# Performance work log

Measured on AMD Instinct MI355X. Metric: run time of the kernel, lower is better.

The kernel has to match this reference:

```python
import jax, jax.numpy as jnp
import numpy as np
from jax import lax

SUB_NO = 20; T_NO = 200; BASIS_NO = 19; T_DATA = 100000; E_NO = 800; I_NO = 200


def make_cos_basis():
    # raised-cosine log-time basis, [BASIS_NO, T_NO]
    i = jnp.arange(BASIS_NO, dtype=jnp.float32)[:, None]
    phi = (jnp.pi / 2.0) * i
    x = jnp.arange(T_NO, dtype=jnp.float32)[None, :]
    raw = 5.0 * jnp.log(x + 1.0)  # cos_scale=5, cos_shift=1
    basis = 0.5 * jnp.cos(raw - phi) + 0.5
    return jnp.where((raw >= phi - jnp.pi) & (raw <= phi + jnp.pi), basis, 0.0)


def causal_group_conv(x, kern):
    # x: [T, sub], kern: [sub, T_no]; out[t,k] = sum_j kern[k,j]*x[t-j,k]
    xr = x.T[None]  # [1, sub, T]
    w = jnp.flip(kern, 1)[:, None, :]  # [sub, 1, T_no]
    out = lax.conv_general_dilated(xr, w, (1,), [(T_NO - 1, 0)],
                                   dimension_numbers=('NCH', 'OIH', 'NCH'),
                                   feature_group_count=kern.shape[0])
    return out[0].T  # [T, sub]


def hist_conv(z, kern):
    # matches torch: pad T_no leading zeros, valid corr with flipped kernel, drop last
    zp = jnp.concatenate([jnp.zeros((T_NO,), z.dtype), z])[None, None, :]
    w = jnp.flip(kern)[None, None, :]
    out = lax.conv_general_dilated(zp, w, (1,), 'VALID',
                                   dimension_numbers=('NCH', 'OIH', 'NCH'))
    return out[0, 0, :-1]  # [T]


def setup_inputs() -> dict:
    key = jax.random.key(0)
    ks = jax.random.split(key, 12)
    # binary dendritic tree: parent of node j is (j-1)//2; C_den[p, j] = 1
    parent = np.maximum((np.arange(SUB_NO) - 1) // 2, 0)
    C_den = np.zeros((SUB_NO, SUB_NO), np.float32)
    for j in range(1, SUB_NO):
        C_den[parent[j], j] = 1.0
    assign_e = jax.random.randint(ks[0], (E_NO,), 0, SUB_NO)
    assign_i = jax.random.randint(ks[1], (I_NO,), 0, SUB_NO)
    C_syn_e = jax.nn.one_hot(assign_e, SUB_NO, dtype=jnp.float32).T
    C_syn_i = jax.nn.one_hot(assign_i, SUB_NO, dtype=jnp.float32).T
    S_e = (jax.random.uniform(ks[2], (T_DATA, E_NO)) < 0.05).astype(jnp.float32)
    S_i = (jax.random.uniform(ks[3], (T_DATA, I_NO)) < 0.05).astype(jnp.float32)
    Z = (jax.random.uniform(ks[4], (T_DATA,)) < 0.02).astype(jnp.float32)
    return {
        'S_e': S_e, 'S_i': S_i, 'Z': Z,
        'C_den': jnp.asarray(C_den), 'C_syn_e': C_syn_e, 'C_syn_i': C_syn_i,
        'W_syn_ns': 0.1 * jax.random.normal(ks[5], (SUB_NO, BASIS_NO, 2)),
        'W_syn_s': 0.1 * jax.random.normal(ks[6], (SUB_NO, BASIS_NO, 2)),
        'W_sub_ns': 0.1 * jnp.ones((SUB_NO,), jnp.float32),
        'W_sub_s': 0.1 * jnp.ones((SUB_NO,), jnp.float32),
        'V_o': jax.random.normal(ks[7], (1,)),
        'Theta_ns': 0.1 * jax.random.normal(ks[8], (SUB_NO,)),
        'Theta_s': 0.1 * jax.random.normal(ks[9], (SUB_NO,)),
        'hist_s_weights': 0.1 * jax.random.normal(ks[10], (BASIS_NO,)),
        'hist_ns_weights': 0.1 * jax.random.normal(ks[11], (BASIS_NO,)),
    }


def reference(S_e, S_i, Z, C_den, C_syn_e, C_syn_i, W_syn_ns, W_syn_s,
              W_sub_ns, W_sub_s, V_o, Theta_ns, Theta_s,
              hist_s_weights, hist_ns_weights):
    cb = make_cos_basis()
    syn_e = S_e @ C_syn_e.T  # [T, sub]
    syn_i = S_i @ C_syn_i.T
    e_kern_ns = W_syn_ns[:, :, 0] @ cb  # [sub, T_no]
    i_kern_ns = W_syn_ns[:, :, 1] @ cb
    e_kern_s = W_syn_s[:, :, 0] @ cb
    i_kern_s = W_syn_s[:, :, 1] @ cb
    syn_ns = causal_group_conv(syn_e, e_kern_ns) + causal_group_conv(syn_i, i_kern_ns)
    syn_s = causal_group_conv(syn_e, e_kern_s) + causal_group_conv(syn_i, i_kern_s)
    ws2 = W_sub_s ** 2
    wns2 = W_sub_ns ** 2
    T = S_e.shape[0]
    s_out = jnp.zeros((T, SUB_NO), syn_s.dtype)
    ns_out = jnp.zeros((T, SUB_NO), syn_ns.dtype)
    # leaf-to-root tree message passing; C_den[k] masks children of node k
    for k in range(SUB_NO - 1, 0, -1):
        mask = C_den[k]
        s_out = s_out.at[:, k].set(jnp.tanh(syn_s[:, k] + s_out @ (mask * ws2) + Theta_s[k]))
        ns_out = ns_out.at[:, k].set(jnp.tanh(syn_ns[:, k] + ns_out @ (mask * wns2) + Theta_ns[k]))
    hist_s_kern = hist_s_weights @ cb  # [T_no]
    hist_ns_kern = hist_ns_weights @ cb
    root_mask = C_den[0]
    final_Z = jax.nn.sigmoid(hist_conv(Z, hist_s_kern) + syn_s[:, 0]
                             + s_out @ (root_mask * ws2) + Theta_s[0])
    root_ns = jnp.tanh(hist_conv(Z, hist_ns_kern) + syn_ns[:, 0]
                       + ns_out @ (root_mask * wns2) + Theta_ns[0])
    final_V = root_ns * wns2[0] + V_o[0]
    out_filters = jnp.vstack([e_kern_ns, i_kern_ns, e_kern_s, i_kern_s,
                              hist_ns_kern[None], hist_s_kern[None]])
    return final_V, final_Z, out_filters
```

## Files before the change

### kernel.cpp

```cpp
#include <hip/hip_runtime.h>
#include <hip/hip_bf16.h>
#include <math.h>

#define SUB_NO 20
#define T_NO   200
#define BASIS_NO 19
#define T_DATA 100000
#define E_NO   800
#define I_NO   200

using u16 = unsigned short;
using u32 = unsigned int;
using u64 = unsigned long long;

__device__ __forceinline__ float bf2f(u16 h) {
  return __builtin_bit_cast(float, (u32)h << 16);
}
__device__ __forceinline__ u16 f2bf(float f) {
  u32 u = __builtin_bit_cast(u32, f);
  u += 0x7FFFu + ((u >> 16) & 1u);
  return (u16)(u >> 16);
}
__device__ __forceinline__ float ldx(const void* p, int i, bool bf) {
  return bf ? bf2f(((const u16*)p)[i]) : ((const float*)p)[i];
}
__device__ __forceinline__ void stx(void* p, int i, float v, bool bf) {
  if (bf) ((u16*)p)[i] = f2bf(v); else ((float*)p)[i] = v;
}

#if defined(__clang__) && (__clang_major__ >= 17) && __has_builtin(__builtin_amdgcn_fdot2_f32_bf16)
typedef __bf16 bf16x2 __attribute__((ext_vector_type(2)));
__device__ __forceinline__ float dot2bf(u32 a, u32 b, float c) {
  return __builtin_amdgcn_fdot2_f32_bf16(__builtin_bit_cast(bf16x2, a),
                                         __builtin_bit_cast(bf16x2, b), c, false);
}
#else
__device__ __forceinline__ float dot2bf(u32 a, u32 b, float c) {
  float ax = __builtin_bit_cast(float, a << 16);
  float ay = __builtin_bit_cast(float, a & 0xFFFF0000u);
  float bx = __builtin_bit_cast(float, b << 16);
  float by = __builtin_bit_cast(float, b & 0xFFFF0000u);
  return fmaf(ay, by, fmaf(ax, bx, c));
}
#endif

#define K0_BLOCKS 21
__global__ __launch_bounds__(256) void k0_prep(
    const u32* __restrict__ probe,
    const void* __restrict__ Wns, const void* __restrict__ Ws,
    const void* __restrict__ hsw, const void* __restrict__ hnsw,
    const void* __restrict__ Cse, const void* __restrict__ Csi,
    u32* __restrict__ kpair, float* __restrict__ hist_s,
    float* __restrict__ hist_ns, int* __restrict__ ae, int* __restrict__ ai,
    void* __restrict__ out) {
  const bool bf = (probe[0] != 0u);
  __shared__ float cb[BASIS_NO * T_NO];
  const int tid = threadIdx.x;
  constexpr float PI = 3.14159265358979323846f;
  for (int idx = tid; idx < BASIS_NO * T_NO; idx += 256) {
    int b = idx / T_NO, j = idx - b * T_NO;
    float phi = 0.5f * PI * (float)b;
    float raw = 5.0f * logf((float)j + 1.0f);
    float v = 0.f;
    if (raw >= phi - PI && raw <= phi + PI) v = 0.5f * cosf(raw - phi) + 0.5f;
    cb[idx] = v;
  }
  __syncthreads();
  const int fbase = 2 * T_DATA;
  for (int gid = blockIdx.x * 256 + tid; gid < 5200; gid += K0_BLOCKS * 256) {
    if (gid < 4000) {
      int k = gid / T_NO, j = gid - k * T_NO;
      float e_ns = 0.f, i_ns = 0.f, e_s = 0.f, i_s = 0.f;
#pragma unroll
      for (int b = 0; b < BASIS_NO; ++b) {
        float c = cb[b * T_NO + j];
        e_ns = fmaf(ldx(Wns, (k * BASIS_NO + b) * 2 + 0, bf), c, e_ns);
        i_ns = fmaf(ldx(Wns, (k * BASIS_NO + b) * 2 + 1, bf), c, i_ns);
        e_s  = fmaf(ldx(Ws,  (k * BASIS_NO + b) * 2 + 0, bf), c, e_s);
        i_s  = fmaf(ldx(Ws,  (k * BASIS_NO + b) * 2 + 1, bf), c, i_s);
      }
      kpair[j * 40 + k]      = (u32)f2bf(e_ns) | ((u32)f2bf(i_ns) << 16);
      kpair[j * 40 + 20 + k] = (u32)f2bf(e_s)  | ((u32)f2bf(i_s)  << 16);
      stx(out, fbase + (0 * SUB_NO + k) * T_NO + j, e_ns, bf);
      stx(out, fbase + (1 * SUB_NO + k) * T_NO + j, i_ns, bf);
      stx(out, fbase + (2 * SUB_NO + k) * T_NO + j, e_s,  bf);
      stx(out, fbase + (3 * SUB_NO + k) * T_NO + j, i_s,  bf);
    } else if (gid < 4200) {
      int j = gid - 4000;
      float hs = 0.f, hns = 0.f;
#pragma unroll
      for (int b = 0; b < BASIS_NO; ++b) {
        float c = cb[b * T_NO + j];
        hs  = fmaf(ldx(hsw,  b, bf), c, hs);
        hns = fmaf(ldx(hnsw, b, bf), c, hns);
      }
      hist_s[j] = hs; hist_ns[j] = hns;
      stx(out, fbase + 80 * T_NO + j, hns, bf);
      stx(out, fbase + 81 * T_NO + j, hs,  bf);
    } else if (gid < 5000) {
      int e = gid - 4200;
      int a = 0;
      for (int k = 0; k < SUB_NO; ++k) if (ldx(Cse, k * E_NO + e, bf) != 0.f) a = k;
      ae[e] = a;
    } else {
      int e = gid - 5000;
      int a = 0;
      for (int k = 0; k < SUB_NO; ++k) if (ldx(Csi, k * I_NO + e, bf) != 0.f) a = k;
      ai[e] = a;
    }
  }
}

#define K1_R 64

__device__ __forceinline__ void k1_load_bf(const void* Se, const void* Si,
                                           int t, int l, uint4& a0, uint4& a1,
                                           uint4& c0) {
  const uint4 z4 = make_uint4(0u, 0u, 0u, 0u);
  const uint4* p = (const uint4*)((const u16*)Se + (size_t)t * E_NO);
  a0 = p[l]; a1 = (l < 36) ? p[64 + l] : z4;
  const uint4* pi = (const uint4*)((const u16*)Si + (size_t)t * I_NO);
  c0 = (l < 25) ? pi[l] : z4;
}

__device__ __forceinline__ void k1_proc_bf(uint4 a0, uint4 a1, uint4 c0,
                                           const u64* rme, const u64* rmi,
                                           int l, int t,
                                           u32* __restrict__ syn_pair) {
  u32 ce = 0, ci = 0;
#pragma unroll
  for (int j = 0; j < 8; ++j) {
    u32 d = (&a0.x)[j >> 1];
    u32 h = (j & 1) ? (d >> 16) : (d & 0xFFFFu);
    u64 m = __ballot(h != 0u);
    ce += (u32)__popcll(rme[j] & m);
  }
#pragma unroll
  for (int j = 0; j < 8; ++j) {
    u32 d = (&a1.x)[j >> 1];
    u32 h = (j & 1) ? (d >> 16) : (d & 0xFFFFu);
    u64 m = __ballot(h != 0u);
    ce += (u32)__popcll(rme[8 + j] & m);
  }
#pragma unroll
  for (int j = 0; j < 8; ++j) {
    u32 d = (&c0.x)[j >> 1];
    u32 h = (j & 1) ? (d >> 16) : (d & 0xFFFFu);
    u64 m = __ballot(h != 0u);
    ci += (u32)__popcll(rmi[j] & m);
  }
  if (l < SUB_NO) {
    u32 pe = (u32)f2bf((float)ce);
    u32 pif = (u32)f2bf((float)ci);
    syn_pair[(size_t)t * SUB_NO + l] = pe | (pif << 16);
  }
}

__global__ __launch_bounds__(256, 4) void k1_agg(
    const u32* __restrict__ probe,
    const void* __restrict__ Se, const void* __restrict__ Si,
    const int* __restrict__ ae, const int* __restrict__ ai,
    u32* __restrict__ syn_pair) {
  const bool bf = (probe[0] != 0u);
  __shared__ u64 mask_e[SUB_NO][16];
  __shared__ u64 mask_i[SUB_NO][8];
  __shared__ int lae[E_NO];
  __shared__ int lai[I_NO];
  const int tid = threadIdx.x;
  const int l = tid & 63;
  const int wv = tid >> 6;
  for (int n = tid; n < E_NO; n += 256) lae[n] = ae[n];
  for (int n = tid; n < I_NO; n += 256) lai[n] = ai[n];
  __syncthreads();
  for (int pid = tid; pid < 480; pid += 256) {
    if (pid < 320) {
      int k = pid >> 4, w = pid & 15;
      u64 m = 0;
      if (bf) {
        if (w < 8) { for (int b = 0; b < 64; ++b) if (lae[8 * b + w] == k) m |= 1ull << b; }
        else       { for (int b = 0; b < 36; ++b) if (lae[512 + 8 * b + (w - 8)] == k) m |= 1ull << b; }
      } else {
        int g = w >> 2, j = w & 3;
        int lim = (g < 3) ? 64 : 8;
        for (int b = 0; b < lim; ++b) if (lae[256 * g + 4 * b + j] == k) m |= 1ull << b;
      }
      mask_e[k][w] = m;
    } else {
      int p2 = pid - 320; int k = p2 >> 3, w = p2 & 7;
      u64 m = 0;
      if (bf) { for (int b = 0; b < 25; ++b) { int e = 8 * b + w; if (e < I_NO && lai[e] == k) m |= 1ull << b; } }
      else if (w < 4) { for (int b = 0; b < 50; ++b) if (lai[4 * b + w] == k) m |= 1ull << b; }
      mask_i[k][w] = m;
    }
  }
  __syncthreads();
  u64 rme[16], rmi[8];
  const int kk = (l < SUB_NO) ? l : 0;
#pragma unroll
  for (int w = 0; w < 16; ++w) rme[w] = mask_e[kk][w];
#pragma unroll
  for (int w = 0; w < 8; ++w) rmi[w] = mask_i[kk][w];

  const int r0 = blockIdx.x * K1_R + wv * 16;
  if (r0 >= T_DATA) return;
  const uint4 z4 = make_uint4(0u, 0u, 0u, 0u);

  if (bf) {
    uint4 A0, A1, C0, B0, B1, D0;
    k1_load_bf(Se, Si, r0, l, A0, A1, C0);
    k1_load_bf(Se, Si, r0 + 1, l, B0, B1, D0);
    for (int i = 0; i < 16; i += 2) {
      uint4 N0 = z4, N1 = z4, M0 = z4, M1 = z4, P0 = z4, Q0 = z4;
      if (i + 2 < 16) {
        k1_load_bf(Se, Si, r0 + i + 2, l, N0, N1, P0);
        k1_load_bf(Se, Si, r0 + i + 3, l, M0, M1, Q0);
      }
      k1_proc_bf(A0, A1, C0, rme, rmi, l, r0 + i, syn_pair);
      k1_proc_bf(B0, B1, D0, rme, rmi, l, r0 + i + 1, syn_pair);
      A0 = N0; A1 = N1; C0 = P0;
      B0 = M0; B1 = M1; D0 = Q0;
    }
  } else {
    uint4 a0, a1, a2, a3, c0;
    {
      const uint4* p = (const uint4*)((const float*)Se + (size_t)r0 * E_NO);
      a0 = p[l]; a1 = p[64 + l]; a2 = p[128 + l]; a3 = (l < 8) ? p[192 + l] : z4;
      const uint4* pi = (const uint4*)((const float*)Si + (size_t)r0 * I_NO);
      c0 = (l < 50) ? pi[l] : z4;
    }
    for (int i = 0; i < 16; ++i) {
      const int t = r0 + i;
      uint4 b0 = z4, b1 = z4, b2 = z4, b3 = z4, d0 = z4;
      if (i + 1 < 16) {
        const uint4* p = (const uint4*)((const float*)Se + (size_t)(t + 1) * E_NO);
        b0 = p[l]; b1 = p[64 + l]; b2 = p[128 + l]; b3 = (l < 8) ? p[192 + l] : z4;
        const uint4* pi = (const uint4*)((const float*)Si + (size_t)(t + 1) * I_NO);
        d0 = (l < 50) ? pi[l] : z4;
      }
      u32 ce = 0, ci = 0;
      const uint4 va[4] = {a0, a1, a2, a3};
#pragma unroll
      for (int g = 0; g < 4; ++g) {
#pragma unroll
        for (int j = 0; j < 4; ++j) {
          u32 d = (&va[g].x)[j];
          u64 m = __ballot(d != 0u);
          ce += (u32)__popcll(rme[4 * g + j] & m);
        }
      }
#pragma unroll
      for (int j = 0; j < 4; ++j) {
        u32 d = (&c0.x)[j];
        u64 m = __ballot(d != 0u);
        ci += (u32)__popcll(rmi[j] & m);
      }
      if (l < SUB_NO) {
        u32 pe = (u32)f2bf((float)ce);
        u32 pif = (u32)f2bf((float)ci);
        syn_pair[(size_t)t * SUB_NO + l] = pe | (pif << 16);
      }
      a0 = b0; a1 = b1; a2 = b2; a3 = b3; c0 = d0;
    }
  }
}

#define K2T  128
#define K2R  (K2T + T_NO)

__global__ __launch_bounds__(320, 6) void k2_conv(
    const u32* __restrict__ probe,
    const u32* __restrict__ syn_pair, const u32* __restrict__ kpair,
    const float* __restrict__ hist_s, const float* __restrict__ hist_ns,
    const void* __restrict__ Z, const void* __restrict__ Wsub_ns,
    const void* __restrict__ Wsub_s, const void* __restrict__ Vo,
    const void* __restrict__ Thns, const void* __restrict__ Ths,
    void* __restrict__ out) {
  const bool bf = (probe[0] != 0u);
  __shared__ __align__(16) unsigned char smem[K2R * SUB_NO * 4];
  uint4* tile4 = (uint4*)smem;
  float* accsh = (float*)smem;
  float* hp    = (float*)(smem + 21000);
  __shared__ float ztile[K2R];
  __shared__ float lhs[T_NO], lhns[T_NO];
  __shared__ float ws2_l[SUB_NO], wns2_l[SUB_NO], ths_l[SUB_NO], thns_l[SUB_NO];
  const int tid = threadIdx.x;
  const int l = tid & 63;
  const int kgu = __builtin_amdgcn_readfirstlane(tid >> 6);
  const int t0 = blockIdx.x * K2T;

  const int base4 = (t0 - T_NO) * (SUB_NO / 4);
  const uint4* sp4 = (const uint4*)syn_pair;
  for (int n = tid; n < K2R * 5; n += 320) {
    int g = base4 + n;
    uint4 v = make_uint4(0u, 0u, 0u, 0u);
    if (g >= 0 && g < T_DATA * SUB_NO / 4) v = sp4[g];
    tile4[n] = v;
  }
  const int zbase = t0 - T_NO;
  for (int n = tid; n < K2R; n += 320) {
    int g = zbase + n;
    ztile[n] = (g >= 0 && g < T_DATA) ? ldx(Z, g, bf) : 0.f;
  }
  for (int n = tid; n < T_NO; n += 320) { lhs[n] = hist_s[n]; lhns[n] = hist_ns[n]; }
  if (tid < SUB_NO) {
    float w = ldx(Wsub_s, tid, bf);   ws2_l[tid]  = w * w;
    float wn = ldx(Wsub_ns, tid, bf); wns2_l[tid] = wn * wn;
    ths_l[tid]  = ldx(Ths, tid, bf);
    thns_l[tid] = ldx(Thns, tid, bf);
  }
  __syncthreads();

  float ans_a[4] = {0,0,0,0}, as_a[4] = {0,0,0,0};
  float ans_b[4] = {0,0,0,0}, as_b[4] = {0,0,0,0};
  float hs_a = 0.f, hns_a = 0.f, hs_b = 0.f, hns_b = 0.f;
  const int mlo = 40 * kgu;

#pragma unroll 2
  for (int m = 0; m < T_NO; ++m) {
    uint4 cns = *(const uint4*)(kpair + m * 40 + 4 * kgu);
    uint4 cs  = *(const uint4*)(kpair + m * 40 + 20 + 4 * kgu);
    uint4 qa = tile4[(l + T_NO - m) * 5 + kgu];
    uint4 qb = tile4[(l + 64 + T_NO - m) * 5 + kgu];
    if ((unsigned)(m - mlo) < 40u) {
      float ls = lhs[m], lns = lhns[m];
      float za = ztile[l + T_NO - 1 - m];
      float zb = ztile[l + 64 + T_NO - 1 - m];
      hs_a = fmaf(ls, za, hs_a);   hns_a = fmaf(lns, za, hns_a);
      hs_b = fmaf(ls, zb, hs_b);   hns_b = fmaf(lns, zb, hns_b);
    }
#pragma unroll
    for (int j = 0; j < 4; ++j) {
      u32 ua = (&qa.x)[j], ub = (&qb.x)[j];
      u32 cn = (&cns.x)[j], c2 = (&cs.x)[j];
      ans_a[j] = dot2bf(ua, cn, ans_a[j]);
      as_a[j]  = dot2bf(ua, c2, as_a[j]);
      ans_b[j] = dot2bf(ub, cn, ans_b[j]);
      as_b[j]  = dot2bf(ub, c2, as_b[j]);
    }
  }
  __syncthreads();

#pragma unroll
  for (int j = 0; j < 4; ++j) {
    const int k = kgu * 4 + j;
    accsh[l * 41 + k]             = as_a[j];
    accsh[l * 41 + 20 + k]        = ans_a[j];
    accsh[(l + 64) * 41 + k]      = as_b[j];
    accsh[(l + 64) * 41 + 20 + k] = ans_b[j];
  }
  float* hp_s = hp;
  float* hp_ns = hp + 640;
  hp_s[kgu * 128 + l] = hs_a;   hp_s[kgu * 128 + 64 + l] = hs_b;
  hp_ns[kgu * 128 + l] = hns_a; hp_ns[kgu * 128 + 64 + l] = hns_b;
  __syncthreads();

  if (kgu < 2) {
    const int tl = kgu * 64 + l;
    float h_s = 0.f, h_ns = 0.f;
#pragma unroll
    for (int w = 0; w < 5; ++w) { h_s += hp_s[w * 128 + tl]; h_ns += hp_ns[w * 128 + tl]; }
    const float* ar = &accsh[tl * 41];
    float so[SUB_NO], no[SUB_NO];
#pragma unroll
    for (int k = SUB_NO - 1; k >= 1; --k) {
      float as_ = ar[k] + ths_l[k];
      float an_ = ar[20 + k] + thns_l[k];
      const int c1 = 2 * k + 1, c2 = 2 * k + 2;
      if (c1 < SUB_NO) { as_ += ws2_l[c1] * so[c1]; an_ += wns2_l[c1] * no[c1]; }
      if (c2 < SUB_NO) { as_ += ws2_l[c2] * so[c2]; an_ += wns2_l[c2] * no[c2]; }
      so[k] = tanhf(as_);
      no[k] = tanhf(an_);
    }
    float zs = h_s + ar[0] + ths_l[0] + ws2_l[1] * so[1] + ws2_l[2] * so[2];
    float zn = h_ns + ar[20] + thns_l[0] + wns2_l[1] * no[1] + wns2_l[2] * no[2];
    float fZ = 1.f / (1.f + expf(-zs));
    float fV = tanhf(zn) * wns2_l[0] + ldx(Vo, 0, bf);
    const int t = t0 + tl;
    if (t < T_DATA) {
      stx(out, t, fV, bf);
      stx(out, T_DATA + t, fZ, bf);
    }
  }
}

extern "C" void kernel_launch(void* const* d_in, const int* in_sizes, int n_in,
                              void* d_out, int out_size, void* d_ws, size_t ws_size,
                              hipStream_t stream) {
  const void* Se      = d_in[0];
  const void* Si      = d_in[1];
  const void* Z       = d_in[2];
  const u32*  probe   = (const u32*)d_in[3];
  const void* Cse     = d_in[4];
  const void* Csi     = d_in[5];
  const void* Wns     = d_in[6];
  const void* Ws_     = d_in[7];
  const void* Wsub_ns = d_in[8];
  const void* Wsub_s  = d_in[9];
  const void* Vo      = d_in[10];
  const void* Thns    = d_in[11];
  const void* Ths     = d_in[12];
  const void* hsw     = d_in[13];
  const void* hnsw    = d_in[14];

  float* wsf      = (float*)d_ws;
  u32*   kpair    = (u32*)wsf;
  float* hist_s   = wsf + 8000;
  float* hist_ns  = wsf + 8200;
  int*   ae       = (int*)(wsf + 8400);
  int*   ai       = (int*)(wsf + 9200);
  u32*   syn_pair = (u32*)(wsf + 9408);

  hipLaunchKernelGGL(k0_prep, dim3(K0_BLOCKS), dim3(256), 0, stream,
                     probe, Wns, Ws_, hsw, hnsw, Cse, Csi,
                     kpair, hist_s, hist_ns, ae, ai, d_out);
  hipLaunchKernelGGL(k1_agg, dim3((T_DATA + K1_R - 1) / K1_R), dim3(256), 0, stream,
                     probe, Se, Si, ae, ai, syn_pair);
  hipLaunchKernelGGL(k2_conv, dim3((T_DATA + K2T - 1) / K2T), dim3(320), 0, stream,
                     probe, syn_pair, kpair, hist_s, hist_ns, Z,
                     Wsub_ns, Wsub_s, Vo, Thns, Ths, d_out);
}
```

Before: 582.0 us.

## Transpose conv smem tile and reuse adjacent time rows via register carry

Each lane now handles two adjacent timesteps (2l, 2l+1) instead of l and l+64. The shared tile is transposed so each sub-group's rows are contiguous, which lets one LDS load per iteration be reused for the neighbouring timestep on the next iteration through a register carry. This halves the shared-memory loads for the synaptic tile in the inner loop, and the unroll factor is raised to 4. The global load pattern in the staging loop becomes strided, and the LDS access stride changes, which could cause bank conflicts.

```diff
diff --git a/kernel.cpp b/kernel.cpp
--- a/kernel.cpp
+++ b/kernel.cpp
@@ -277,7 +277,7 @@
     void* __restrict__ out) {
   const bool bf = (probe[0] != 0u);
   __shared__ __align__(16) unsigned char smem[K2R * SUB_NO * 4];
-  uint4* tile4 = (uint4*)smem;
+  uint4* tileT = (uint4*)smem;
   float* accsh = (float*)smem;
   float* hp    = (float*)(smem + 21000);
   __shared__ float ztile[K2R];
@@ -288,13 +288,13 @@
   const int kgu = __builtin_amdgcn_readfirstlane(tid >> 6);
   const int t0 = blockIdx.x * K2T;
 
-  const int base4 = (t0 - T_NO) * (SUB_NO / 4);
   const uint4* sp4 = (const uint4*)syn_pair;
-  for (int n = tid; n < K2R * 5; n += 320) {
-    int g = base4 + n;
+  for (int n = tid; n < 5 * K2R; n += 320) {
+    int kgt = n / K2R, row = n - kgt * K2R;
+    int g = t0 - T_NO + row;
     uint4 v = make_uint4(0u, 0u, 0u, 0u);
-    if (g >= 0 && g < T_DATA * SUB_NO / 4) v = sp4[g];
-    tile4[n] = v;
+    if (g >= 0 && g < T_DATA) v = sp4[g * 5 + kgt];
+    tileT[kgt * K2R + row] = v;
   }
   const int zbase = t0 - T_NO;
   for (int n = tid; n < K2R; n += 320) {
@@ -314,44 +314,47 @@
   float ans_b[4] = {0,0,0,0}, as_b[4] = {0,0,0,0};
   float hs_a = 0.f, hns_a = 0.f, hs_b = 0.f, hns_b = 0.f;
   const int mlo = 40 * kgu;
-
-#pragma unroll 2
+  const uint4* myrow = &tileT[kgu * K2R + 2 * l];
+
+  uint4 carry = myrow[T_NO + 1];
+
+#pragma unroll 4
   for (int m = 0; m < T_NO; ++m) {
+    uint4 fresh = myrow[T_NO - m];
     uint4 cns = *(const uint4*)(kpair + m * 40 + 4 * kgu);
     uint4 cs  = *(const uint4*)(kpair + m * 40 + 20 + 4 * kgu);
-    uint4 qa = tile4[(l + T_NO - m) * 5 + kgu];
-    uint4 qb = tile4[(l + 64 + T_NO - m) * 5 + kgu];
     if ((unsigned)(m - mlo) < 40u) {
       float ls = lhs[m], lns = lhns[m];
-      float za = ztile[l + T_NO - 1 - m];
-      float zb = ztile[l + 64 + T_NO - 1 - m];
+      float za = ztile[2 * l + T_NO - 1 - m];
+      float zb = ztile[2 * l + T_NO - m];
       hs_a = fmaf(ls, za, hs_a);   hns_a = fmaf(lns, za, hns_a);
       hs_b = fmaf(ls, zb, hs_b);   hns_b = fmaf(lns, zb, hns_b);
     }
 #pragma unroll
     for (int j = 0; j < 4; ++j) {
-      u32 ua = (&qa.x)[j], ub = (&qb.x)[j];
+      u32 ua = (&fresh.x)[j], ub = (&carry.x)[j];
       u32 cn = (&cns.x)[j], c2 = (&cs.x)[j];
       ans_a[j] = dot2bf(ua, cn, ans_a[j]);
       as_a[j]  = dot2bf(ua, c2, as_a[j]);
       ans_b[j] = dot2bf(ub, cn, ans_b[j]);
       as_b[j]  = dot2bf(ub, c2, as_b[j]);
     }
+    carry = fresh;
   }
   __syncthreads();
 
 #pragma unroll
   for (int j = 0; j < 4; ++j) {
     const int k = kgu * 4 + j;
-    accsh[l * 41 + k]             = as_a[j];
-    accsh[l * 41 + 20 + k]        = ans_a[j];
-    accsh[(l + 64) * 41 + k]      = as_b[j];
-    accsh[(l + 64) * 41 + 20 + k] = ans_b[j];
+    accsh[(2 * l) * 41 + k]          = as_a[j];
+    accsh[(2 * l) * 41 + 20 + k]     = ans_a[j];
+    accsh[(2 * l + 1) * 41 + k]      = as_b[j];
+    accsh[(2 * l + 1) * 41 + 20 + k] = ans_b[j];
   }
   float* hp_s = hp;
   float* hp_ns = hp + 640;
-  hp_s[kgu * 128 + l] = hs_a;   hp_s[kgu * 128 + 64 + l] = hs_b;
-  hp_ns[kgu * 128 + l] = hns_a; hp_ns[kgu * 128 + 64 + l] = hns_b;
+  hp_s[kgu * 128 + 2 * l] = hs_a;   hp_s[kgu * 128 + 2 * l + 1] = hs_b;
+  hp_ns[kgu * 128 + 2 * l] = hns_a; hp_ns[kgu * 128 + 2 * l + 1] = hns_b;
   __syncthreads();
 
   if (kgu < 2) {
```

Measured after the change: 579.8 us. About the same (-0.4%).
